# Kernel optimization log

Measured on AMD Instinct MI355X. Metric: run time of the kernel, lower is better.

Reference implementation:

```python
import jax, jax.numpy as jnp
import numpy as np

SLOPE = 0.01  # LeakyReLU default negative slope


def grid_sample2d(image, grid):
    """Bilinear, padding_mode='border', align_corners=True.
    image: [B,C,H,W], grid: [B,h,w,2] in [-1,1]. Returns [B,C,h,w]."""
    B, C, H, W = image.shape
    _, h, w, _ = grid.shape
    ix = (grid[..., 0] + 1) / 2 * (W - 1)  # [B,h,w]
    iy = (grid[..., 1] + 1) / 2 * (H - 1)
    ix0 = jnp.floor(ix)
    iy0 = jnp.floor(iy)
    # bilinear weights (computed from unclamped corner coords, as in source)
    nw = (ix0 + 1 - ix) * (iy0 + 1 - iy)
    ne = (ix - ix0) * (iy0 + 1 - iy)
    sw = (ix0 + 1 - ix) * (iy - iy0)
    se = (ix - ix0) * (iy - iy0)
    x0 = jnp.clip(ix0.astype(jnp.int32), 0, W - 1)
    x1 = jnp.clip(ix0.astype(jnp.int32) + 1, 0, W - 1)
    y0 = jnp.clip(iy0.astype(jnp.int32), 0, H - 1)
    y1 = jnp.clip(iy0.astype(jnp.int32) + 1, 0, H - 1)
    img = image.reshape(B, C, H * W)

    def gather(yi, xi):
        idx = (yi * W + xi).reshape(B, 1, h * w)
        idx = jnp.broadcast_to(idx, (B, C, h * w))
        return jnp.take_along_axis(img, idx, axis=2).reshape(B, C, h, w)

    out = (gather(y0, x0) * nw[:, None] + gather(y0, x1) * ne[:, None]
           + gather(y1, x0) * sw[:, None] + gather(y1, x1) * se[:, None])
    return out


def leaky_relu(x):
    return jnp.where(x >= 0, x, SLOPE * x)


def setup_inputs() -> dict:
    key = jax.random.key(0)
    ks = jax.random.split(key, 10)
    B, C, H, W = 1, 32, 512, 512
    h, w = 2048, 512
    hid, out_dim = 32, 4
    inp = {
        "xy": jax.random.normal(ks[0], (B, C, H, W), jnp.float32),
        "xz": jax.random.normal(ks[1], (B, C, H, W), jnp.float32),
        "yz": jax.random.normal(ks[2], (B, C, H, W), jnp.float32),
        "coords": jax.random.uniform(ks[3], (B, h, w, 3), jnp.float32, -1.0, 1.0),
        "gauss_mat": jax.random.normal(ks[4], (3, 16), jnp.float32),
        "W0": jax.random.normal(ks[5], (C + 32, C), jnp.float32) * 0.1,
        "b0": jnp.zeros((C,), jnp.float32),
        "W1": jax.random.normal(ks[6], (C, hid), jnp.float32) * 0.1,
        "b1": jnp.zeros((hid,), jnp.float32),
        "W2": jax.random.normal(ks[7], (hid, hid), jnp.float32) * 0.1,
        "b2": jnp.zeros((hid,), jnp.float32),
        "W3": jax.random.normal(ks[8], (hid, out_dim), jnp.float32) * 0.1,
        "b3": jnp.zeros((out_dim,), jnp.float32),
    }
    return inp


def reference(xy, xz, yz, coords, gauss_mat, W0, b0, W1, b1, W2, b2, W3, b3):
    e1 = grid_sample2d(xy, coords[..., jnp.array([0, 1])])
    e2 = grid_sample2d(xz, coords[..., jnp.array([0, 2])])
    e3 = grid_sample2d(yz, coords[..., jnp.array([1, 2])])
    x = (e1 + e2 + e3) / 3.0  # [B,C,h,w]
    x = jnp.moveaxis(x, 1, -1)  # [B,h,w,C]
    # positional encoding
    p = coords * (2.0 * jnp.pi)
    proj = jnp.einsum('bhwd,dc->bhwc', p, gauss_mat)  # [B,h,w,16]
    pos_emb = jnp.concatenate([jnp.sin(proj), jnp.cos(proj)], axis=-1)  # [B,h,w,32]
    x = leaky_relu(jnp.concatenate([x, pos_emb], axis=-1) @ W0 + b0)
    x = leaky_relu(x @ W1 + b1)
    x = leaky_relu(x @ W2 + b2)
    x = x @ W3 + b3
    return x
```

## Files before the change

kernel.cpp:

```cpp
#include <hip/hip_runtime.h>
#include <hip/hip_fp16.h>

#define HW_ (512 * 512)
#define NPIX (2048 * 512)
#define NBIN 4096
#define SORT_BLOCKS 256
#define PXPT 16

typedef _Float16 half_t;
typedef __attribute__((ext_vector_type(8))) _Float16 half8;
typedef __attribute__((ext_vector_type(2))) _Float16 half2v;
typedef __attribute__((ext_vector_type(4))) float f32x4;
typedef unsigned int uint;

__device__ __forceinline__ half8 splat8(float w)
{
    half_t h = (half_t)w;
    half8 r = {h, h, h, h, h, h, h, h};
    return r;
}

__device__ __forceinline__ uint packh(float lo, float hi)
{
    half_t l = (half_t)lo, h = (half_t)hi;
    unsigned short lb = __builtin_bit_cast(unsigned short, l);
    unsigned short hb = __builtin_bit_cast(unsigned short, h);
    return (uint)lb | ((uint)hb << 16);
}

__device__ __forceinline__ uint pkrtz_u32(float lo, float hi)
{
    return __builtin_bit_cast(uint, __builtin_amdgcn_cvt_pkrtz(lo, hi));
}

__device__ __forceinline__ float lky(float x) { return x >= 0.f ? x : 0.01f * x; }

__device__ __forceinline__ uint pk_lky_u32(float a, float b)
{
    uint h = pkrtz_u32(a, b);
    half2v v = __builtin_bit_cast(half2v, h);
    half2v c = {(half_t)0.01f, (half_t)0.01f};
    half2v m = __builtin_elementwise_max(v, v * c);
    return __builtin_bit_cast(uint, m);
}

__device__ __forceinline__ unsigned spread4(int v)
{
    return (v & 1) | ((v & 2) << 2) | ((v & 4) << 4) | ((v & 8) << 6);
}

__device__ __forceinline__ unsigned bin_of(float cx, float cy, float cz)
{
    int qx = min(max((int)((cx + 1.f) * 8.f), 0), 15);
    int qy = min(max((int)((cy + 1.f) * 8.f), 0), 15);
    int qz = min(max((int)((cz + 1.f) * 8.f), 0), 15);
    return spread4(qx) | (spread4(qy) << 1) | (spread4(qz) << 2);
}

__global__ __launch_bounds__(256) void hist_k(const float* __restrict__ coords,
                                              unsigned* __restrict__ hist)
{
    __shared__ unsigned lcnt[NBIN];
    int t = threadIdx.x;
#pragma unroll
    for (int i = 0; i < NBIN / 256; ++i) lcnt[i * 256 + t] = 0;
    __syncthreads();
    int base = blockIdx.x * (PXPT * 256);
#pragma unroll
    for (int i = 0; i < PXPT; ++i) {
        int px = base + i * 256 + t;
        float cx = coords[(size_t)px * 3 + 0];
        float cy = coords[(size_t)px * 3 + 1];
        float cz = coords[(size_t)px * 3 + 2];
        atomicAdd(&lcnt[bin_of(cx, cy, cz)], 1u);
    }
    __syncthreads();
#pragma unroll
    for (int i = 0; i < NBIN / 256; ++i) {
        uint v = lcnt[i * 256 + t];
        if (v) atomicAdd(&hist[i * 256 + t], v);
    }
}

__global__ __launch_bounds__(256) void scan_k(const unsigned* __restrict__ hist,
                                              unsigned* __restrict__ ofs)
{
    __shared__ unsigned part[256];
    int t = threadIdx.x;
    unsigned loc[16], s = 0;
#pragma unroll
    for (int i = 0; i < 16; ++i) { loc[i] = s; s += hist[t * 16 + i]; }
    part[t] = s;
    __syncthreads();
    for (int d = 1; d < 256; d <<= 1) {
        unsigned v = (t >= d) ? part[t - d] : 0u;
        __syncthreads();
        part[t] += v;
        __syncthreads();
    }
    unsigned base = (t == 0) ? 0u : part[t - 1];
#pragma unroll
    for (int i = 0; i < 16; ++i) ofs[t * 16 + i] = base + loc[i];
}

__global__ __launch_bounds__(256) void big_k(
    const float* __restrict__ xy, const float* __restrict__ xz,
    const float* __restrict__ yz, half_t* __restrict__ tp,
    const float* __restrict__ coords, unsigned* __restrict__ ofs,
    float4* __restrict__ sorted,
    const float* __restrict__ W0, const float* __restrict__ W1,
    const float* __restrict__ W2, const float* __restrict__ W3,
    const float* __restrict__ b0, const float* __restrict__ b1,
    const float* __restrict__ b2, const float* __restrict__ b3,
    uint* __restrict__ wfrag, float* __restrict__ bb)
{
    __shared__ __align__(16) uint sh[8192];
    int b = blockIdx.x;
    int t = threadIdx.x;

    if (b < 12288) {
        half_t (*tile)[68] = (half_t(*)[68])sh;
        int xc = b & 7;
        int y  = (b >> 3) & 511;
        int p  = b >> 12;
        const float* __restrict__ src = (p == 0) ? xy : (p == 1) ? xz : yz;
#pragma unroll
        for (int i = 0; i < 8; ++i) {
            int e  = i * 256 + t;
            int c  = e >> 6;
            int xl = e & 63;
            tile[c][xl] = (half_t)src[(size_t)c * HW_ + y * 512 + xc * 64 + xl];
        }
        __syncthreads();
        half_t* __restrict__ dst = tp + ((size_t)p * HW_ + y * 512 + xc * 64) * 32;
#pragma unroll
        for (int i = 0; i < 8; ++i) {
            int e  = i * 256 + t;
            int c  = e & 31;
            int xl = e >> 5;
            dst[(size_t)xl * 32 + c] = tile[c][xl];
        }
    } else if (b < 12288 + SORT_BLOCKS) {
        uint* lcnt  = sh;
        uint* lbase = sh + NBIN;
#pragma unroll
        for (int i = 0; i < NBIN / 256; ++i) lcnt[i * 256 + t] = 0;
        __syncthreads();
        int base = (b - 12288) * (PXPT * 256);
        uint sav[PXPT];
#pragma unroll
        for (int i = 0; i < PXPT; ++i) {
            int px = base + i * 256 + t;
            float cx = coords[(size_t)px * 3 + 0];
            float cy = coords[(size_t)px * 3 + 1];
            float cz = coords[(size_t)px * 3 + 2];
            unsigned bn = bin_of(cx, cy, cz);
            unsigned r  = atomicAdd(&lcnt[bn], 1u);
            sav[i] = (bn << 16) | r;
        }
        __syncthreads();
#pragma unroll
        for (int i = 0; i < NBIN / 256; ++i) {
            uint v = lcnt[i * 256 + t];
            lbase[i * 256 + t] = v ? atomicAdd(&ofs[i * 256 + t], v) : 0u;
        }
        __syncthreads();
#pragma unroll
        for (int i = 0; i < PXPT; ++i) {
            int px = base + i * 256 + t;
            float cx = coords[(size_t)px * 3 + 0];
            float cy = coords[(size_t)px * 3 + 1];
            float cz = coords[(size_t)px * 3 + 2];
            unsigned bn = sav[i] >> 16, r = sav[i] & 0xffffu;
            sorted[lbase[bn] + r] = make_float4(cx, cy, cz, __uint_as_float((uint)px));
        }
    } else {
        int tid = (b - 12288 - SORT_BLOCKS) * 256 + t;
        if (tid < 2304) {
            int f = tid >> 8, rem = tid & 255;
            int l = rem >> 2, u = rem & 3;
            int jl = l & 15, g = l >> 4;
            float lo, hi;
            if (f < 4) {
                int t_ = f >> 1, c = f & 1;
                int j  = t_ * 16 + jl;
                int k0 = 32 * c + 8 * g + 2 * u;
                float sc = c ? 1.f : (1.f / 3.f);
                lo = W0[k0 * 32 + j] * sc;
                hi = W0[(k0 + 1) * 32 + j] * sc;
            } else if (f < 8) {
                const float* W = (f < 6) ? W1 : W2;
                int t_ = f & 1;
                int j  = t_ * 16 + jl;
                int klo = (u < 2) ? (4 * g + 2 * u) : (16 + 4 * g + 2 * u - 4);
                lo = W[klo * 32 + j];
                hi = W[(klo + 1) * 32 + j];
            } else {
                int klo = (u < 2) ? (4 * g + 2 * u) : (16 + 4 * g + 2 * u - 4);
                lo = (jl < 4) ? W3[klo * 4 + jl] : 0.f;
                hi = (jl < 4) ? W3[(klo + 1) * 4 + jl] : 0.f;
            }
            wfrag[tid] = packh(lo, hi);
        } else if (tid < 2304 + 112) {
            int u = tid - 2304;
            float v;
            if (u < 32)      v = b0[u];
            else if (u < 64) v = b1[u - 32];
            else if (u < 96) v = b2[u - 64];
            else             v = (u - 96 < 4) ? b3[u - 96] : 0.f;
            bb[u] = v;
        }
    }
}

__device__ __forceinline__ void axis1d(float gc, int& i0, int& i1, float& tf)
{
    float ic = fmaf(gc, 255.5f, 255.5f);
    float fc = floorf(ic);
    tf = ic - fc;
    int c0 = (int)fc;
    i0 = min(max(c0, 0), 511);
    i1 = min(max(c0 + 1, 0), 511);
}

__device__ __forceinline__ void interp_q(const half_t* __restrict__ pl,
                                         int i00, int i01, int i10, int i11,
                                         float tc, float tr, int ch, half8& acc)
{
    const half_t* __restrict__ p = pl + ch * 8;
    half8 a = *(const half8*)(p + (size_t)i00 * 32);
    half8 b = *(const half8*)(p + (size_t)i01 * 32);
    half8 c = *(const half8*)(p + (size_t)i10 * 32);
    half8 d = *(const half8*)(p + (size_t)i11 * 32);
    float w00 = (1.f - tc) * (1.f - tr);
    float w01 = tc * (1.f - tr);
    float w10 = (1.f - tc) * tr;
    float w11 = tc * tr;
    acc = acc + a * splat8(w00) + b * splat8(w01) + c * splat8(w10) + d * splat8(w11);
}

__device__ __forceinline__ void corners(float gx, float gy,
                                        int& i00, int& i01, int& i10, int& i11,
                                        float& wnw, float& wne, float& wsw, float& wse)
{
    int x0, x1, y0, y1; float tx, ty;
    axis1d(gx, x0, x1, tx);
    axis1d(gy, y0, y1, ty);
    i00 = y0 * 512 + x0;
    i01 = y0 * 512 + x1;
    i10 = y1 * 512 + x0;
    i11 = y1 * 512 + x1;
    wnw = (1.f - tx) * (1.f - ty);
    wne = tx * (1.f - ty);
    wsw = (1.f - tx) * ty;
    wse = tx * ty;
}

__global__ __launch_bounds__(256) void decoder_fused_k(
    const half_t* __restrict__ tp, const float4* __restrict__ sorted,
    const float* __restrict__ gauss, const uint* __restrict__ wfrag,
    const float* __restrict__ bb, float* __restrict__ out)
{
    __shared__ __align__(16) char act0[4][8192];
    const int t  = threadIdx.x;
    const int l  = t & 63;
    const int wv = t >> 6;
    char* base = act0[wv];
    const int jl = l & 15, g = l >> 4;
    const int ch = l & 3;
    const int pq = l >> 2;

    int b   = blockIdx.x;
    int swz = (b & 7) * 512 + (b >> 3);
    int j   = (swz * 4 + wv) * 64 + l;

    float4 s = sorted[j];
    uint idreg = __float_as_uint(s.w);
    float cx = s.x, cy = s.y, cz = s.z;

#pragma unroll
    for (int q = 0; q < 4; ++q) {
        int pp = q * 16 + pq;
        float gx = __shfl(cx, pp);
        float gy = __shfl(cy, pp);
        float gz = __shfl(cz, pp);
        int x0, x1, y0, y1, z0, z1;
        float tx, ty, tz;
        axis1d(gx, x0, x1, tx);
        axis1d(gy, y0, y1, ty);
        axis1d(gz, z0, z1, tz);
        half8 accq = {};
        interp_q(tp,
                 y0 * 512 + x0, y0 * 512 + x1, y1 * 512 + x0, y1 * 512 + x1,
                 tx, ty, ch, accq);
        interp_q(tp + (size_t)HW_ * 32,
                 z0 * 512 + x0, z0 * 512 + x1, z1 * 512 + x0, z1 * 512 + x1,
                 tx, tz, ch, accq);
        interp_q(tp + (size_t)2 * HW_ * 32,
                 z0 * 512 + y0, z0 * 512 + y1, z1 * 512 + y0, z1 * 512 + y1,
                 ty, tz, ch, accq);
        *(half8*)(base + (pp << 7) + ((ch ^ (pp & 7)) << 4)) = accq;
    }

    half8 wf[9];
#pragma unroll
    for (int f = 0; f < 9; ++f) {
        uint4 u = *(const uint4*)(wfrag + f * 256 + l * 4);
        wf[f] = __builtin_bit_cast(half8, u);
    }
    f32x4 bv0a = *(const f32x4*)(bb +  0 + g * 4);
    f32x4 bv0b = *(const f32x4*)(bb + 16 + g * 4);
    f32x4 bv1a = *(const f32x4*)(bb + 32 + g * 4);
    f32x4 bv1b = *(const f32x4*)(bb + 48 + g * 4);
    f32x4 bv2a = *(const f32x4*)(bb + 64 + g * 4);
    f32x4 bv2b = *(const f32x4*)(bb + 80 + g * 4);
    f32x4 bv3  = *(const f32x4*)(bb + 96 + g * 4);

    const float TWO_PI = 6.283185307179586f;
    float px = cx * TWO_PI, py = cy * TWO_PI, pz = cz * TWO_PI;
    float sn[16], cs[16];
#pragma unroll
    for (int c = 0; c < 16; ++c) {
        float pr = px * gauss[c] + py * gauss[16 + c] + pz * gauss[32 + c];
        sn[c] = __sinf(pr);
        cs[c] = __cosf(pr);
    }
    half8 pc[4];
#pragma unroll
    for (int i = 0; i < 8; ++i) {
        pc[0][i] = (half_t)sn[i];     pc[1][i] = (half_t)sn[8 + i];
        pc[2][i] = (half_t)cs[i];     pc[3][i] = (half_t)cs[8 + i];
    }
#pragma unroll
    for (int c = 0; c < 4; ++c)
        *(half8*)(base + (l << 7) + (((4 + c) ^ (l & 7)) << 4)) = pc[c];

#pragma unroll
    for (int pt = 0; pt < 4; ++pt) {
        int p = pt * 16 + jl;
        half8 Ba = *(const half8*)(base + (p << 7) + ((g ^ (p & 7)) << 4));
        half8 Bb = *(const half8*)(base + (p << 7) + (((4 + g) ^ (p & 7)) << 4));

        f32x4 d0 = bv0a, d1 = bv0b;
        d0 = __builtin_amdgcn_mfma_f32_16x16x32_f16(wf[0], Ba, d0, 0, 0, 0);
        d0 = __builtin_amdgcn_mfma_f32_16x16x32_f16(wf[1], Bb, d0, 0, 0, 0);
        d1 = __builtin_amdgcn_mfma_f32_16x16x32_f16(wf[2], Ba, d1, 0, 0, 0);
        d1 = __builtin_amdgcn_mfma_f32_16x16x32_f16(wf[3], Bb, d1, 0, 0, 0);
        uint4 u1;
        u1.x = pk_lky_u32(d0[0], d0[1]);
        u1.y = pk_lky_u32(d0[2], d0[3]);
        u1.z = pk_lky_u32(d1[0], d1[1]);
        u1.w = pk_lky_u32(d1[2], d1[3]);
        half8 B1 = __builtin_bit_cast(half8, u1);

        d0 = bv1a; d1 = bv1b;
        d0 = __builtin_amdgcn_mfma_f32_16x16x32_f16(wf[4], B1, d0, 0, 0, 0);
        d1 = __builtin_amdgcn_mfma_f32_16x16x32_f16(wf[5], B1, d1, 0, 0, 0);
        uint4 u2;
        u2.x = pk_lky_u32(d0[0], d0[1]);
        u2.y = pk_lky_u32(d0[2], d0[3]);
        u2.z = pk_lky_u32(d1[0], d1[1]);
        u2.w = pk_lky_u32(d1[2], d1[3]);
        half8 B2 = __builtin_bit_cast(half8, u2);

        d0 = bv2a; d1 = bv2b;
        d0 = __builtin_amdgcn_mfma_f32_16x16x32_f16(wf[6], B2, d0, 0, 0, 0);
        d1 = __builtin_amdgcn_mfma_f32_16x16x32_f16(wf[7], B2, d1, 0, 0, 0);
        uint4 u3;
        u3.x = pk_lky_u32(d0[0], d0[1]);
        u3.y = pk_lky_u32(d0[2], d0[3]);
        u3.z = pk_lky_u32(d1[0], d1[1]);
        u3.w = pk_lky_u32(d1[2], d1[3]);
        half8 B3 = __builtin_bit_cast(half8, u3);

        f32x4 d3 = bv3;
        d3 = __builtin_amdgcn_mfma_f32_16x16x32_f16(wf[8], B3, d3, 0, 0, 0);
        int gid = __shfl((int)idreg, pt * 16 + (l & 15));
        if (l < 16) {
            *(f32x4*)(out + (size_t)(uint)gid * 4) = d3;
        }
    }
}

__device__ __forceinline__ void sample_dir(const float* __restrict__ pl,
                                           float gx, float gy, float* __restrict__ acc)
{
    int i00, i01, i10, i11;
    float wnw, wne, wsw, wse;
    corners(gx, gy, i00, i01, i10, i11, wnw, wne, wsw, wse);
#pragma unroll
    for (int c = 0; c < 32; ++c) {
        const float* __restrict__ bq = pl + (size_t)c * HW_;
        acc[c] += wnw * bq[i00] + wne * bq[i01] + wsw * bq[i10] + wse * bq[i11];
    }
}

__global__ __launch_bounds__(256) void decoder_fb_k(
    const float* __restrict__ xy, const float* __restrict__ xz,
    const float* __restrict__ yz,
    const float* __restrict__ coords, const float* __restrict__ gauss,
    const float* __restrict__ W0, const float* __restrict__ b0,
    const float* __restrict__ W1, const float* __restrict__ b1,
    const float* __restrict__ W2, const float* __restrict__ b2,
    const float* __restrict__ W3, const float* __restrict__ b3,
    float* __restrict__ out)
{
    int pix = blockIdx.x * 256 + threadIdx.x;
    float cx = coords[(size_t)pix * 3 + 0];
    float cy = coords[(size_t)pix * 3 + 1];
    float cz = coords[(size_t)pix * 3 + 2];

    float act[64];
#pragma unroll
    for (int i = 0; i < 32; ++i) act[i] = 0.f;
    sample_dir(xy, cx, cy, act);
    sample_dir(xz, cx, cz, act);
    sample_dir(yz, cy, cz, act);
#pragma unroll
    for (int i = 0; i < 32; ++i) act[i] *= (1.f / 3.f);

    const float TWO_PI = 6.283185307179586f;
    float px = cx * TWO_PI, py = cy * TWO_PI, pz = cz * TWO_PI;
#pragma unroll
    for (int c = 0; c < 16; ++c) {
        float pr = px * gauss[c] + py * gauss[16 + c] + pz * gauss[32 + c];
        act[32 + c] = __sinf(pr);
        act[48 + c] = __cosf(pr);
    }

    float h[32];
#pragma unroll
    for (int jj = 0; jj < 32; ++jj) h[jj] = b0[jj];
#pragma unroll
    for (int k = 0; k < 64; ++k) {
        float a = act[k];
#pragma unroll
        for (int jj = 0; jj < 32; ++jj) h[jj] = fmaf(a, W0[k * 32 + jj], h[jj]);
    }
#pragma unroll
    for (int jj = 0; jj < 32; ++jj) act[jj] = lky(h[jj]);
#pragma unroll
    for (int jj = 0; jj < 32; ++jj) h[jj] = b1[jj];
#pragma unroll
    for (int k = 0; k < 32; ++k) {
        float a = act[k];
#pragma unroll
        for (int jj = 0; jj < 32; ++jj) h[jj] = fmaf(a, W1[k * 32 + jj], h[jj]);
    }
#pragma unroll
    for (int jj = 0; jj < 32; ++jj) act[jj] = lky(h[jj]);
#pragma unroll
    for (int jj = 0; jj < 32; ++jj) h[jj] = b2[jj];
#pragma unroll
    for (int k = 0; k < 32; ++k) {
        float a = act[k];
#pragma unroll
        for (int jj = 0; jj < 32; ++jj) h[jj] = fmaf(a, W2[k * 32 + jj], h[jj]);
    }
#pragma unroll
    for (int jj = 0; jj < 32; ++jj) act[jj] = lky(h[jj]);
    float o[4];
#pragma unroll
    for (int jj = 0; jj < 4; ++jj) o[jj] = b3[jj];
#pragma unroll
    for (int k = 0; k < 32; ++k) {
        float a = act[k];
#pragma unroll
        for (int jj = 0; jj < 4; ++jj) o[jj] = fmaf(a, W3[k * 4 + jj], o[jj]);
    }
    *(float4*)(out + (size_t)pix * 4) = make_float4(o[0], o[1], o[2], o[3]);
}

extern "C" void kernel_launch(void* const* d_in, const int* in_sizes, int n_in,
                              void* d_out, int out_size, void* d_ws, size_t ws_size,
                              hipStream_t stream)
{
    const float* xy     = (const float*)d_in[0];
    const float* xz     = (const float*)d_in[1];
    const float* yz     = (const float*)d_in[2];
    const float* coords = (const float*)d_in[3];
    const float* gauss  = (const float*)d_in[4];
    const float* W0     = (const float*)d_in[5];
    const float* b0     = (const float*)d_in[6];
    const float* W1     = (const float*)d_in[7];
    const float* b1     = (const float*)d_in[8];
    const float* W2     = (const float*)d_in[9];
    const float* b2     = (const float*)d_in[10];
    const float* W3     = (const float*)d_in[11];
    const float* b3     = (const float*)d_in[12];
    float* out = (float*)d_out;

    const size_t plane_bytes = (size_t)3 * HW_ * 32 * sizeof(half_t);
    const size_t hist_off    = plane_bytes;
    const size_t ofs_off     = hist_off + NBIN * 4;
    const size_t wfrag_off   = ofs_off + NBIN * 4;
    const size_t bb_off      = wfrag_off + 12288;
    const size_t sorted_off  = bb_off + 4096;
    const size_t need_fused  = sorted_off + (size_t)NPIX * sizeof(float4);
    const int npix_blocks    = NPIX / 256;

    if (ws_size >= need_fused) {
        half_t*   tp     = (half_t*)d_ws;
        unsigned* hist   = (unsigned*)((char*)d_ws + hist_off);
        unsigned* ofs    = (unsigned*)((char*)d_ws + ofs_off);
        uint*     wfrag  = (uint*)((char*)d_ws + wfrag_off);
        float*    bb     = (float*)((char*)d_ws + bb_off);
        float4*   sorted = (float4*)((char*)d_ws + sorted_off);

        (void)hipMemsetAsync(hist, 0, NBIN * 4, stream);
        hist_k<<<SORT_BLOCKS, 256, 0, stream>>>(coords, hist);
        scan_k<<<1, 256, 0, stream>>>(hist, ofs);
        big_k<<<12288 + SORT_BLOCKS + 10, 256, 0, stream>>>(
            xy, xz, yz, tp, coords, ofs, sorted,
            W0, W1, W2, W3, b0, b1, b2, b3, wfrag, bb);
        decoder_fused_k<<<npix_blocks, 256, 0, stream>>>(
            tp, sorted, gauss, wfrag, bb, out);
    } else {
        decoder_fb_k<<<npix_blocks, 256, 0, stream>>>(
            xy, xz, yz, coords, gauss,
            W0, b0, W1, b1, W2, b2, W3, b3, out);
    }
}
```

Measured before the change: 142.1 us.

## Fold histogram into transpose kernel, split scatter out, shrink decoder blocks

The histogram pass is merged into the plane-transpose kernel, so its blocks overlap with the transpose work instead of running as a separate launch. The scatter step moves into its own kernel after the scan, and it keeps the coords in registers instead of reloading them. The decoder now runs 128-thread blocks with half the LDS, and its block swizzle is adjusted to match, which should raise occupancy. The trade-off is that the scatter is now serialized after the big kernel, and there are still five stream operations.

```diff
diff --git a/kernel.cpp b/kernel.cpp
--- a/kernel.cpp
+++ b/kernel.cpp
@@ -57,64 +57,17 @@
     return spread4(qx) | (spread4(qy) << 1) | (spread4(qz) << 2);
 }
 
-__global__ __launch_bounds__(256) void hist_k(const float* __restrict__ coords,
-                                              unsigned* __restrict__ hist)
-{
-    __shared__ unsigned lcnt[NBIN];
-    int t = threadIdx.x;
-#pragma unroll
-    for (int i = 0; i < NBIN / 256; ++i) lcnt[i * 256 + t] = 0;
-    __syncthreads();
-    int base = blockIdx.x * (PXPT * 256);
-#pragma unroll
-    for (int i = 0; i < PXPT; ++i) {
-        int px = base + i * 256 + t;
-        float cx = coords[(size_t)px * 3 + 0];
-        float cy = coords[(size_t)px * 3 + 1];
-        float cz = coords[(size_t)px * 3 + 2];
-        atomicAdd(&lcnt[bin_of(cx, cy, cz)], 1u);
-    }
-    __syncthreads();
-#pragma unroll
-    for (int i = 0; i < NBIN / 256; ++i) {
-        uint v = lcnt[i * 256 + t];
-        if (v) atomicAdd(&hist[i * 256 + t], v);
-    }
-}
-
-__global__ __launch_bounds__(256) void scan_k(const unsigned* __restrict__ hist,
-                                              unsigned* __restrict__ ofs)
-{
-    __shared__ unsigned part[256];
-    int t = threadIdx.x;
-    unsigned loc[16], s = 0;
-#pragma unroll
-    for (int i = 0; i < 16; ++i) { loc[i] = s; s += hist[t * 16 + i]; }
-    part[t] = s;
-    __syncthreads();
-    for (int d = 1; d < 256; d <<= 1) {
-        unsigned v = (t >= d) ? part[t - d] : 0u;
-        __syncthreads();
-        part[t] += v;
-        __syncthreads();
-    }
-    unsigned base = (t == 0) ? 0u : part[t - 1];
-#pragma unroll
-    for (int i = 0; i < 16; ++i) ofs[t * 16 + i] = base + loc[i];
-}
-
 __global__ __launch_bounds__(256) void big_k(
     const float* __restrict__ xy, const float* __restrict__ xz,
     const float* __restrict__ yz, half_t* __restrict__ tp,
-    const float* __restrict__ coords, unsigned* __restrict__ ofs,
-    float4* __restrict__ sorted,
+    const float* __restrict__ coords, unsigned* __restrict__ hist,
     const float* __restrict__ W0, const float* __restrict__ W1,
     const float* __restrict__ W2, const float* __restrict__ W3,
     const float* __restrict__ b0, const float* __restrict__ b1,
     const float* __restrict__ b2, const float* __restrict__ b3,
     uint* __restrict__ wfrag, float* __restrict__ bb)
 {
-    __shared__ __align__(16) uint sh[8192];
+    __shared__ __align__(16) uint sh[4096];
     int b = blockIdx.x;
     int t = threadIdx.x;
 
@@ -141,38 +94,24 @@
             dst[(size_t)xl * 32 + c] = tile[c][xl];
         }
     } else if (b < 12288 + SORT_BLOCKS) {
-        uint* lcnt  = sh;
-        uint* lbase = sh + NBIN;
+        uint* lcnt = sh;
 #pragma unroll
         for (int i = 0; i < NBIN / 256; ++i) lcnt[i * 256 + t] = 0;
         __syncthreads();
         int base = (b - 12288) * (PXPT * 256);
-        uint sav[PXPT];
 #pragma unroll
         for (int i = 0; i < PXPT; ++i) {
             int px = base + i * 256 + t;
             float cx = coords[(size_t)px * 3 + 0];
             float cy = coords[(size_t)px * 3 + 1];
             float cz = coords[(size_t)px * 3 + 2];
-            unsigned bn = bin_of(cx, cy, cz);
-            unsigned r  = atomicAdd(&lcnt[bn], 1u);
-            sav[i] = (bn << 16) | r;
+            atomicAdd(&lcnt[bin_of(cx, cy, cz)], 1u);
         }
         __syncthreads();
 #pragma unroll
         for (int i = 0; i < NBIN / 256; ++i) {
             uint v = lcnt[i * 256 + t];
-            lbase[i * 256 + t] = v ? atomicAdd(&ofs[i * 256 + t], v) : 0u;
-        }
-        __syncthreads();
-#pragma unroll
-        for (int i = 0; i < PXPT; ++i) {
-            int px = base + i * 256 + t;
-            float cx = coords[(size_t)px * 3 + 0];
-            float cy = coords[(size_t)px * 3 + 1];
-            float cz = coords[(size_t)px * 3 + 2];
-            unsigned bn = sav[i] >> 16, r = sav[i] & 0xffffu;
-            sorted[lbase[bn] + r] = make_float4(cx, cy, cz, __uint_as_float((uint)px));
+            if (v) atomicAdd(&hist[i * 256 + t], v);
         }
     } else {
         int tid = (b - 12288 - SORT_BLOCKS) * 256 + t;
@@ -213,6 +152,68 @@
     }
 }
 
+__global__ __launch_bounds__(256) void scan_k(const unsigned* __restrict__ hist,
+                                              unsigned* __restrict__ ofs)
+{
+    __shared__ unsigned part[256];
+    int t = threadIdx.x;
+    unsigned loc[16], s = 0;
+#pragma unroll
+    for (int i = 0; i < 16; ++i) { loc[i] = s; s += hist[t * 16 + i]; }
+    part[t] = s;
+    __syncthreads();
+    for (int d = 1; d < 256; d <<= 1) {
+        unsigned v = (t >= d) ? part[t - d] : 0u;
+        __syncthreads();
+        part[t] += v;
+        __syncthreads();
+    }
+    unsigned base = (t == 0) ? 0u : part[t - 1];
+#pragma unroll
+    for (int i = 0; i < 16; ++i) ofs[t * 16 + i] = base + loc[i];
+}
+
+__global__ __launch_bounds__(256) void scatter_k(const float* __restrict__ coords,
+                                                 unsigned* __restrict__ ofs,
+                                                 float4* __restrict__ sorted)
+{
+    __shared__ unsigned lcnt[NBIN];
+    __shared__ unsigned lbase[NBIN];
+    int t = threadIdx.x;
+#pragma unroll
+    for (int i = 0; i < NBIN / 256; ++i) lcnt[i * 256 + t] = 0;
+    __syncthreads();
+
+    int base = blockIdx.x * (PXPT * 256);
+    float cxv[PXPT], cyv[PXPT], czv[PXPT];
+    uint sav[PXPT];
+#pragma unroll
+    for (int i = 0; i < PXPT; ++i) {
+        int px = base + i * 256 + t;
+        cxv[i] = coords[(size_t)px * 3 + 0];
+        cyv[i] = coords[(size_t)px * 3 + 1];
+        czv[i] = coords[(size_t)px * 3 + 2];
+        unsigned bn = bin_of(cxv[i], cyv[i], czv[i]);
+        unsigned r  = atomicAdd(&lcnt[bn], 1u);
+        sav[i] = (bn << 16) | r;
+    }
+    __syncthreads();
+#pragma unroll
+    for (int i = 0; i < NBIN / 256; ++i) {
+        uint v = lcnt[i * 256 + t];
+        lbase[i * 256 + t] = v ? atomicAdd(&ofs[i * 256 + t], v) : 0u;
+    }
+    __syncthreads();
+
+#pragma unroll
+    for (int i = 0; i < PXPT; ++i) {
+        int px = base + i * 256 + t;
+        unsigned bn = sav[i] >> 16, r = sav[i] & 0xffffu;
+        sorted[lbase[bn] + r] = make_float4(cxv[i], cyv[i], czv[i],
+                                            __uint_as_float((uint)px));
+    }
+}
+
 __device__ __forceinline__ void axis1d(float gc, int& i0, int& i1, float& tf)
 {
     float ic = fmaf(gc, 255.5f, 255.5f);
@@ -256,12 +257,12 @@
     wse = tx * ty;
 }
 
-__global__ __launch_bounds__(256) void decoder_fused_k(
+__global__ __launch_bounds__(128) void decoder_fused_k(
     const half_t* __restrict__ tp, const float4* __restrict__ sorted,
     const float* __restrict__ gauss, const uint* __restrict__ wfrag,
     const float* __restrict__ bb, float* __restrict__ out)
 {
-    __shared__ __align__(16) char act0[4][8192];
+    __shared__ __align__(16) char act0[2][8192];
     const int t  = threadIdx.x;
     const int l  = t & 63;
     const int wv = t >> 6;
@@ -271,8 +272,8 @@
     const int pq = l >> 2;
 
     int b   = blockIdx.x;
-    int swz = (b & 7) * 512 + (b >> 3);
-    int j   = (swz * 4 + wv) * 64 + l;
+    int swz = (b & 7) * 1024 + (b >> 3);
+    int j   = (swz * 2 + wv) * 64 + l;
 
     float4 s = sorted[j];
     uint idreg = __float_as_uint(s.w);
@@ -497,7 +498,6 @@
     const size_t bb_off      = wfrag_off + 12288;
     const size_t sorted_off  = bb_off + 4096;
     const size_t need_fused  = sorted_off + (size_t)NPIX * sizeof(float4);
-    const int npix_blocks    = NPIX / 256;
 
     if (ws_size >= need_fused) {
         half_t*   tp     = (half_t*)d_ws;
@@ -508,15 +508,15 @@
         float4*   sorted = (float4*)((char*)d_ws + sorted_off);
 
         (void)hipMemsetAsync(hist, 0, NBIN * 4, stream);
-        hist_k<<<SORT_BLOCKS, 256, 0, stream>>>(coords, hist);
+        big_k<<<12288 + SORT_BLOCKS + 10, 256, 0, stream>>>(
+            xy, xz, yz, tp, coords, hist,
+            W0, W1, W2, W3, b0, b1, b2, b3, wfrag, bb);
         scan_k<<<1, 256, 0, stream>>>(hist, ofs);
-        big_k<<<12288 + SORT_BLOCKS + 10, 256, 0, stream>>>(
-            xy, xz, yz, tp, coords, ofs, sorted,
-            W0, W1, W2, W3, b0, b1, b2, b3, wfrag, bb);
-        decoder_fused_k<<<npix_blocks, 256, 0, stream>>>(
+        scatter_k<<<SORT_BLOCKS, 256, 0, stream>>>(coords, ofs, sorted);
+        decoder_fused_k<<<NPIX / 128, 128, 0, stream>>>(
             tp, sorted, gauss, wfrag, bb, out);
     } else {
-        decoder_fb_k<<<npix_blocks, 256, 0, stream>>>(
+        decoder_fb_k<<<NPIX / 256, 256, 0, stream>>>(
             xy, xz, yz, coords, gauss,
             W0, b0, W1, b1, W2, b2, W3, b3, out);
     }
```

New measurement: 137.3 us. 3.4% less time.
